# Performance work log

Measured on AMD Instinct MI355X. Metric: run time of the kernel, lower is better.

## Reference

```python
import jax, jax.numpy as jnp
import numpy as np

B, D, L, N, M, K = 256, 512, 196, 1024, 512, 10000  # batch, context, num_ctx, hidden, embed, vocab


def setup_inputs() -> dict:
    key = jax.random.key(0)
    ks = jax.random.split(key, 20)
    r = lambda k, s: jax.random.normal(k, s, dtype=jnp.float32) * 0.02
    return {
        "a_i": jax.random.normal(ks[0], (B, D, L), dtype=jnp.float32),
        "inp": jax.random.normal(ks[1], (B, 1, K), dtype=jnp.float32),
        "hn_prev": jax.random.normal(ks[2], (B, 1, N), dtype=jnp.float32),
        "cn_prev": jax.random.normal(ks[3], (B, 1, N), dtype=jnp.float32),
        "f_att_w": r(ks[4], (N + D,)),  # Linear(n+D -> 1), stored as a vector
        "f_att_b": r(ks[5], (1,)),
        "gate_w": r(ks[6], (N,)),       # Linear(n -> 1)
        "gate_b": r(ks[7], (1,)),
        "E_w": r(ks[8], (M, K)),        # torch Linear weight [out, in]
        "E_b": r(ks[9], (M,)),
        "W_ih": r(ks[10], (4 * N, D + N + M)),  # LSTM input->hidden (i,f,g,o)
        "W_hh": r(ks[11], (4 * N, N)),
        "b_ih": r(ks[12], (4 * N,)),
        "b_hh": r(ks[13], (4 * N,)),
        "Lh_w": r(ks[14], (M, N)),
        "Lh_b": r(ks[15], (M,)),
        "Lz_w": r(ks[16], (M, D)),
        "Lz_b": r(ks[17], (M,)),
        "Lo_w": r(ks[18], (K, M)),
        "Lo_b": r(ks[19], (K,)),
    }


def reference(a_i, inp, hn_prev, cn_prev,
              f_att_w, f_att_b, gate_w, gate_b,
              E_w, E_b, W_ih, W_hh, b_ih, b_hh,
              Lh_w, Lh_b, Lz_w, Lz_b, Lo_w, Lo_b):
    h = hn_prev[:, 0]  # [B, N]
    c = cn_prev[:, 0]  # [B, N]
    # --- additive attention: the 196-iteration torch loop batched into one einsum ---
    # cat((a_i[:,:,i], h)) @ f_att_w splits into the a-part and h-part of the weight.
    w_a, w_h = f_att_w[:D], f_att_w[D:]
    e = jnp.einsum('bdl,d->bl', a_i, w_a) + (h @ w_h)[:, None] + f_att_b  # [B, L]
    alpha = jax.nn.softmax(e, axis=1)                                     # [B, L]
    beta = jax.nn.sigmoid(h @ gate_w + gate_b)                            # [B]
    z = beta[:, None] * jnp.einsum('bl,bdl->bd', alpha, a_i)              # [B, D]
    # --- word embedding ---
    w_emb = inp[:, 0] @ E_w.T + E_b                                       # [B, M]
    # --- single-step LSTM (PyTorch gate order i, f, g, o) ---
    x = jnp.concatenate([w_emb, h, z], axis=1)                            # [B, M+N+D]
    gates = x @ W_ih.T + b_ih + h @ W_hh.T + b_hh                         # [B, 4N]
    i_g, f_g, g_g, o_g = jnp.split(gates, 4, axis=1)
    cn = jax.nn.sigmoid(f_g) * c + jax.nn.sigmoid(i_g) * jnp.tanh(g_g)
    hn = jax.nn.sigmoid(o_g) * jnp.tanh(cn)
    # --- output projection ---
    deep_out = w_emb + (hn @ Lh_w.T + Lh_b) + (z @ Lz_w.T + Lz_b)         # [B, M]
    p_yt = deep_out @ Lo_w.T + Lo_b                                       # [B, K]
    return (p_yt[:, None, :], hn[:, None, :], cn[:, None, :], alpha[:, None, :])
```

## Files before the change

### kernel.cpp

```cpp
#include <hip/hip_runtime.h>
#include <hip/hip_bf16.h>
#include <math.h>

#define BB 256
#define DD 512
#define LL 196
#define NN 1024
#define MM 512
#define KK 10000

#define OUT_PY 0
#define OUT_HN ((size_t)2560000)
#define OUT_CN ((size_t)2822144)
#define OUT_AL ((size_t)3084288)

#define OFF_PE     ((size_t)0)
#define OFF_BETA   ((size_t)802816)
#define OFF_Z      ((size_t)803072)
#define OFF_EMB    ((size_t)934144)
#define OFF_DEEP   ((size_t)1065216)
#define OFF_EMBP   ((size_t)1196288)
#define OFF_GATESP ((size_t)5390592)
#define OFF_DP     ((size_t)13779200)

typedef __attribute__((ext_vector_type(8))) short short8v;
typedef __attribute__((ext_vector_type(4))) float f32x4;

__device__ __forceinline__ unsigned short f2bf(float f) {
    unsigned int u = __builtin_bit_cast(unsigned int, f);
    u += 0x7fffu + ((u >> 16) & 1u);
    return (unsigned short)(u >> 16);
}

__device__ __forceinline__ void gl_lds16(const float* g, float* l) {
    __builtin_amdgcn_global_load_lds(
        (const __attribute__((address_space(1))) void*)g,
        (__attribute__((address_space(3))) void*)l, 16, 0, 0);
}

__device__ __forceinline__ short8v stage8(const float* __restrict__ p, bool ok,
                                          int kbase, int Ktot) {
    short8v v;
    if (ok && (kbase + 7 < Ktot)) {
        const float4 x = *(const float4*)(p + kbase);
        const float4 y = *(const float4*)(p + kbase + 4);
        v[0] = (short)f2bf(x.x); v[1] = (short)f2bf(x.y);
        v[2] = (short)f2bf(x.z); v[3] = (short)f2bf(x.w);
        v[4] = (short)f2bf(y.x); v[5] = (short)f2bf(y.y);
        v[6] = (short)f2bf(y.z); v[7] = (short)f2bf(y.w);
    } else {
#pragma unroll
        for (int i = 0; i < 8; ++i) {
            const int k = kbase + i;
            v[i] = (short)f2bf((ok && k < Ktot) ? p[k] : 0.f);
        }
    }
    return v;
}

struct GSrc { const float* A; int lda; const float* B; int ldb; int ktn; int K; };

__device__ __forceinline__ void gemm_body(
    const int bx, const int by, const int bz, const int rowBlocks,
    const GSrc s1, const GSrc s2,
    float* __restrict__ C, const int ldc, const int Ncols,
    const int ktPerSplit, const float* __restrict__ bias,
    short (*As)[64][72], short (*Bs)[64][72])
{
    const int t = threadIdx.x;
    const int row0 = bx * 64;
    const int col0 = by * 64;
    const int ktTot = s1.ktn + s2.ktn;
    const int kt0 = bz * ktPerSplit;
    const int nk = min(ktTot, kt0 + ktPerSplit) - kt0;

    const int sr = t >> 2;
    const int sk = (t & 3) << 4;
    const int bc = col0 + sr;
    const bool bok = (bc < Ncols);
    const float* aP1 = s1.A + (size_t)(row0 + sr) * s1.lda;
    const float* bP1 = s1.B + (size_t)(bok ? bc : 0) * s1.ldb;
    const float* aP2 = s2.A ? (s2.A + (size_t)(row0 + sr) * s2.lda) : aP1;
    const float* bP2 = s2.A ? (s2.B + (size_t)(bok ? bc : 0) * s2.ldb) : bP1;

    const int l = t & 63, w = t >> 6;
    const int wrow = (w >> 1) * 32, wcol = (w & 1) * 32;
    const int lr = l & 15, g = l >> 4, g8 = g * 8;

    f32x4 acc[2][2] = {};

    short8v sa0, sa1, sb0, sb1;
    {
        const int ktg = kt0;
        const float* aR; const float* bR; int kk, Kt;
        if (ktg < s1.ktn) { aR = aP1; bR = bP1; kk = (ktg << 6) + sk; Kt = s1.K; }
        else              { aR = aP2; bR = bP2; kk = ((ktg - s1.ktn) << 6) + sk; Kt = s2.K; }
        sa0 = stage8(aR, true, kk, Kt);  sa1 = stage8(aR, true, kk + 8, Kt);
        sb0 = stage8(bR, bok,  kk, Kt);  sb1 = stage8(bR, bok,  kk + 8, Kt);
    }
    *(short8v*)&As[0][sr][sk] = sa0; *(short8v*)&As[0][sr][sk + 8] = sa1;
    *(short8v*)&Bs[0][sr][sk] = sb0; *(short8v*)&Bs[0][sr][sk + 8] = sb1;
    __syncthreads();

    int cur = 0;
    for (int kt = 0; kt < nk; ++kt) {
        const bool more = (kt + 1 < nk);
        if (more) {
            const int ktg = kt0 + kt + 1;
            const float* aR; const float* bR; int kk, Kt;
            if (ktg < s1.ktn) { aR = aP1; bR = bP1; kk = (ktg << 6) + sk; Kt = s1.K; }
            else              { aR = aP2; bR = bP2; kk = ((ktg - s1.ktn) << 6) + sk; Kt = s2.K; }
            sa0 = stage8(aR, true, kk, Kt);  sa1 = stage8(aR, true, kk + 8, Kt);
            sb0 = stage8(bR, bok,  kk, Kt);  sb1 = stage8(bR, bok,  kk + 8, Kt);
        }
#pragma unroll
        for (int ks = 0; ks < 2; ++ks) {
            const int ko = ks * 32 + g8;
            short8v a0 = *(const short8v*)&As[cur][wrow + lr][ko];
            short8v a1 = *(const short8v*)&As[cur][wrow + 16 + lr][ko];
            short8v b0 = *(const short8v*)&Bs[cur][wcol + lr][ko];
            short8v b1 = *(const short8v*)&Bs[cur][wcol + 16 + lr][ko];
            acc[0][0] = __builtin_amdgcn_mfma_f32_16x16x32_bf16(a0, b0, acc[0][0], 0, 0, 0);
            acc[0][1] = __builtin_amdgcn_mfma_f32_16x16x32_bf16(a0, b1, acc[0][1], 0, 0, 0);
            acc[1][0] = __builtin_amdgcn_mfma_f32_16x16x32_bf16(a1, b0, acc[1][0], 0, 0, 0);
            acc[1][1] = __builtin_amdgcn_mfma_f32_16x16x32_bf16(a1, b1, acc[1][1], 0, 0, 0);
        }
        if (more) {
            *(short8v*)&As[cur ^ 1][sr][sk] = sa0;
            *(short8v*)&As[cur ^ 1][sr][sk + 8] = sa1;
            *(short8v*)&Bs[cur ^ 1][sr][sk] = sb0;
            *(short8v*)&Bs[cur ^ 1][sr][sk + 8] = sb1;
        }
        __syncthreads();
        cur ^= 1;
    }

    float* Cp = C + (size_t)bz * ((size_t)rowBlocks * 64) * ldc;
#pragma unroll
    for (int m = 0; m < 2; ++m)
#pragma unroll
        for (int n = 0; n < 2; ++n)
#pragma unroll
            for (int j = 0; j < 4; ++j) {
                const int r = row0 + wrow + m * 16 + g * 4 + j;
                const int c = col0 + wcol + n * 16 + lr;
                if (c < Ncols) {
                    float v = acc[m][n][j];
                    if (bias) v += bias[c];
                    Cp[(size_t)r * ldc + c] = v;
                }
            }
}

__global__ __launch_bounds__(256) void att_e_slab(
    const float* __restrict__ a_i, const float* __restrict__ f_att_w,
    float* __restrict__ pe)
{
    __shared__ __align__(16) float slab[6280];
    const int t = threadIdx.x;
    const int b = blockIdx.x >> 4, ch = blockIdx.x & 15;
    const int w = t >> 6, lane = t & 63;
    const float* gbase = a_i + ((size_t)b * DD + ch * 32) * LL;
#pragma unroll
    for (int k = 0; k < 7; ++k) {
        const int cw = k * 256 + w * 64;
        if (cw + lane < 1568)
            gl_lds16(gbase + (size_t)(cw + lane) * 4, slab + (size_t)cw * 4);
    }
    if (t < 8) slab[6272 + t] = 0.f;
    asm volatile("s_waitcnt vmcnt(0)" ::: "memory");
    __syncthreads();
    if (t < LL) {
        const float* wp = f_att_w + ch * 32;
        float e = 0.f;
#pragma unroll
        for (int d = 0; d < 32; ++d) e += slab[d * LL + t] * wp[d];
        pe[((size_t)b * 16 + ch) * LL + t] = e;
    }
}

__global__ __launch_bounds__(256) void att_z_slab(
    const float* __restrict__ a_i, const float* __restrict__ alpha,
    const float* __restrict__ beta, float* __restrict__ z)
{
    __shared__ __align__(16) float slab[6280];
    __shared__ float al[200];
    const int t = threadIdx.x;
    const int b = blockIdx.x >> 4, ch = blockIdx.x & 15;
    const int w = t >> 6, lane = t & 63;
    const float* gbase = a_i + ((size_t)b * DD + ch * 32) * LL;
#pragma unroll
    for (int k = 0; k < 7; ++k) {
        const int cw = k * 256 + w * 64;
        if (cw + lane < 1568)
            gl_lds16(gbase + (size_t)(cw + lane) * 4, slab + (size_t)cw * 4);
    }
    if (t < 200) al[t] = (t < LL) ? alpha[(size_t)b * LL + t] : 0.f;
    if (t < 8) slab[6272 + t] = 0.f;
    asm volatile("s_waitcnt vmcnt(0)" ::: "memory");
    __syncthreads();
    const int r = t >> 3, q = t & 7;
    const float* rowp = slab + r * LL + q * 25;
    const float* alq  = al + q * 25;
    float s = 0.f;
#pragma unroll
    for (int j = 0; j < 25; ++j) s += rowp[j] * alq[j];
    s += __shfl_xor(s, 1, 64);
    s += __shfl_xor(s, 2, 64);
    s += __shfl_xor(s, 4, 64);
    if (q == 0) z[(size_t)b * DD + ch * 32 + r] = beta[b] * s;
}

__global__ __launch_bounds__(256) void l2_emb_gatesh(
    const float* __restrict__ inp, const float* __restrict__ E_w,
    float* __restrict__ embp,
    const float* __restrict__ h, const float* __restrict__ W_ih,
    const float* __restrict__ W_hh, float* __restrict__ gatesp)
{
    __shared__ __align__(16) short As[2][64][72];
    __shared__ __align__(16) short Bs[2][64][72];
    const int bid = blockIdx.x;
    if (bid < 1024) {
        GSrc s1 = {inp, KK, E_w, KK, 157, KK};
        GSrc s2 = {nullptr, 0, nullptr, 0, 0, 0};
        gemm_body(bid & 3, (bid >> 2) & 7, bid >> 5, 4, s1, s2,
                  embp, MM, MM, 5, nullptr, As, Bs);
    } else {
        const int i = bid - 1024;
        GSrc s1 = {h, NN, W_ih + 512, 2048, 16, NN};
        GSrc s2 = {h, NN, W_hh, NN, 16, NN};
        gemm_body(i & 3, (i >> 2) & 63, i >> 8, 4, s1, s2,
                  gatesp, 4096, 4096, 8, nullptr, As, Bs);
    }
}

__global__ __launch_bounds__(256) void l3_softmax_embred(
    const float* __restrict__ pe, const float* __restrict__ h,
    const float* __restrict__ f_att_w, const float* __restrict__ f_att_b,
    const float* __restrict__ gate_w, const float* __restrict__ gate_b,
    float* __restrict__ alpha_out, float* __restrict__ beta,
    const float* __restrict__ embp, const float* __restrict__ E_b,
    float* __restrict__ emb)
{
    const int bid = blockIdx.x;
    const int t = threadIdx.x;
    if (bid < 256) {
        const int b = bid;
        __shared__ float red[256];
        __shared__ float red2[256];
        const float4 h4 = *(const float4*)(h + (size_t)b * NN + t * 4);
        const float4 w4 = *(const float4*)(f_att_w + DD + t * 4);
        const float4 g4 = *(const float4*)(gate_w + t * 4);
        float hd = h4.x * w4.x + h4.y * w4.y + h4.z * w4.z + h4.w * w4.w;
        float gd = h4.x * g4.x + h4.y * g4.y + h4.z * g4.z + h4.w * g4.w;
        red[t] = hd; red2[t] = gd;
        __syncthreads();
        for (int s = 128; s > 0; s >>= 1) {
            if (t < s) { red[t] += red[t + s]; red2[t] += red2[t + s]; }
            __syncthreads();
        }
        const float hdot = red[0];
        const float gdot = red2[0];
        __syncthreads();
        float e = -3.4e38f;
        if (t < LL) {
            const float* p = pe + (size_t)b * 16 * LL + t;
            e = hdot + f_att_b[0];
#pragma unroll
            for (int ch = 0; ch < 16; ++ch) e += p[ch * LL];
        }
        red[t] = e;
        __syncthreads();
        for (int s = 128; s > 0; s >>= 1) {
            if (t < s) red[t] = fmaxf(red[t], red[t + s]);
            __syncthreads();
        }
        const float mx = red[0];
        __syncthreads();
        const float ex = (t < LL) ? expf(e - mx) : 0.f;
        red[t] = ex;
        __syncthreads();
        for (int s = 128; s > 0; s >>= 1) {
            if (t < s) red[t] += red[t + s];
            __syncthreads();
        }
        const float inv = 1.f / red[0];
        if (t < LL) alpha_out[(size_t)b * LL + t] = ex * inv;
        if (t == 0) beta[b] = 1.f / (1.f + expf(-(gdot + gate_b[0])));
    } else {
        const int idx = (bid - 256) * 256 + t;
        const int j = idx & 511;
        float v = E_b[j];
#pragma unroll
        for (int s = 0; s < 32; ++s) v += embp[(size_t)s * (BB * 512) + idx];
        emb[idx] = v;
    }
}

__global__ __launch_bounds__(256) void l5_gatesez_lz(
    const float* __restrict__ emb, const float* __restrict__ z,
    const float* __restrict__ W_ih, float* __restrict__ gatesp,
    const float* __restrict__ Lz_w, float* __restrict__ dp)
{
    __shared__ __align__(16) short As[2][64][72];
    __shared__ __align__(16) short Bs[2][64][72];
    const int bid = blockIdx.x;
    if (bid < 512) {
        GSrc s1 = {emb, MM, W_ih, 2048, 8, MM};
        GSrc s2 = {nullptr, 0, nullptr, 0, 0, 0};
        gemm_body(bid & 3, (bid >> 2) & 63, bid >> 8, 4, s1, s2,
                  gatesp + (size_t)4 * BB * 4096, 4096, 4096, 4, nullptr, As, Bs);
    } else if (bid < 1024) {
        const int i = bid - 512;
        GSrc s1 = {z, DD, W_ih + 1536, 2048, 8, DD};
        GSrc s2 = {nullptr, 0, nullptr, 0, 0, 0};
        gemm_body(i & 3, (i >> 2) & 63, i >> 8, 4, s1, s2,
                  gatesp + (size_t)6 * BB * 4096, 4096, 4096, 4, nullptr, As, Bs);
    } else {
        const int i = bid - 1024;
        GSrc s1 = {z, DD, Lz_w, DD, 8, DD};
        GSrc s2 = {nullptr, 0, nullptr, 0, 0, 0};
        gemm_body(i & 3, (i >> 2) & 7, i >> 5, 4, s1, s2,
                  dp, MM, MM, 1, nullptr, As, Bs);
    }
}

__global__ __launch_bounds__(256) void l6_lstm(
    const float* __restrict__ gatesp,
    const float* __restrict__ b_ih, const float* __restrict__ b_hh,
    const float* __restrict__ c_prev, float* __restrict__ hn, float* __restrict__ cn)
{
    const int idx = blockIdx.x * 256 + threadIdx.x;
    const int b = idx >> 10, n = idx & 1023;
    float g[4];
#pragma unroll
    for (int gi = 0; gi < 4; ++gi) {
        const int col = gi * 1024 + n;
        const size_t o = (size_t)b * 4096 + col;
        float v = b_ih[col] + b_hh[col];
#pragma unroll
        for (int s = 0; s < 8; ++s) v += gatesp[(size_t)s * (BB * 4096) + o];
        g[gi] = v;
    }
    const float si = 1.f / (1.f + expf(-g[0]));
    const float sf = 1.f / (1.f + expf(-g[1]));
    const float so = 1.f / (1.f + expf(-g[3]));
    const float tg = tanhf(g[2]);
    const float c = c_prev[idx];
    const float cnv = sf * c + si * tg;
    const float hnv = so * tanhf(cnv);
    cn[idx] = cnv;
    hn[idx] = hnv;
}

__global__ __launch_bounds__(256) void l7_lh(
    const float* __restrict__ hn, const float* __restrict__ Lh_w,
    float* __restrict__ dp_hi)
{
    __shared__ __align__(16) short As[2][64][72];
    __shared__ __align__(16) short Bs[2][64][72];
    const int bid = blockIdx.x;
    GSrc s1 = {hn, NN, Lh_w, NN, 16, NN};
    GSrc s2 = {nullptr, 0, nullptr, 0, 0, 0};
    gemm_body(bid & 3, (bid >> 2) & 7, bid >> 5, 4, s1, s2,
              dp_hi, MM, MM, 1, nullptr, As, Bs);
}

__global__ __launch_bounds__(256) void l8_deep(
    const float* __restrict__ emb, const float* __restrict__ dp,
    const float* __restrict__ Lh_b, const float* __restrict__ Lz_b,
    float* __restrict__ deep)
{
    const int idx = blockIdx.x * 256 + threadIdx.x;
    const int j = idx & 511;
    float v = emb[idx] + Lh_b[j] + Lz_b[j];
#pragma unroll
    for (int s = 0; s < 24; ++s) v += dp[(size_t)s * (BB * 512) + idx];
    deep[idx] = v;
}

__global__ __launch_bounds__(256) void l9_pyt(
    const float* __restrict__ deep, const float* __restrict__ Lo_w,
    const float* __restrict__ Lo_b, float* __restrict__ out)
{
    __shared__ __align__(16) short As[2][64][72];
    __shared__ __align__(16) short Bs[2][64][72];
    const int bid = blockIdx.x;
    GSrc s1 = {deep, MM, Lo_w, MM, 8, MM};
    GSrc s2 = {nullptr, 0, nullptr, 0, 0, 0};
    gemm_body(bid & 3, bid >> 2, 0, 4, s1, s2,
              out, KK, KK, 8, Lo_b, As, Bs);
}

extern "C" void kernel_launch(void* const* d_in, const int* in_sizes, int n_in,
                              void* d_out, int out_size, void* d_ws, size_t ws_size,
                              hipStream_t stream)
{
    const float* a_i     = (const float*)d_in[0];
    const float* inp     = (const float*)d_in[1];
    const float* hn_prev = (const float*)d_in[2];
    const float* cn_prev = (const float*)d_in[3];
    const float* f_att_w = (const float*)d_in[4];
    const float* f_att_b = (const float*)d_in[5];
    const float* gate_w  = (const float*)d_in[6];
    const float* gate_b  = (const float*)d_in[7];
    const float* E_w     = (const float*)d_in[8];
    const float* E_b     = (const float*)d_in[9];
    const float* W_ih    = (const float*)d_in[10];
    const float* W_hh    = (const float*)d_in[11];
    const float* b_ih    = (const float*)d_in[12];
    const float* b_hh    = (const float*)d_in[13];
    const float* Lh_w    = (const float*)d_in[14];
    const float* Lh_b    = (const float*)d_in[15];
    const float* Lz_w    = (const float*)d_in[16];
    const float* Lz_b    = (const float*)d_in[17];
    const float* Lo_w    = (const float*)d_in[18];
    const float* Lo_b    = (const float*)d_in[19];

    float* out = (float*)d_out;
    float* ws  = (float*)d_ws;

    float* PE     = ws + OFF_PE;
    float* BETA   = ws + OFF_BETA;
    float* Z      = ws + OFF_Z;
    float* EMB    = ws + OFF_EMB;
    float* DEEP   = ws + OFF_DEEP;
    float* EMBP   = ws + OFF_EMBP;
    float* GATESP = ws + OFF_GATESP;
    float* DP     = ws + OFF_DP;

    att_e_slab<<<4096, 256, 0, stream>>>(a_i, f_att_w, PE);

    l2_emb_gatesh<<<2048, 256, 0, stream>>>(inp, E_w, EMBP,
                                            hn_prev, W_ih, W_hh, GATESP);

    l3_softmax_embred<<<768, 256, 0, stream>>>(PE, hn_prev, f_att_w, f_att_b,
                                               gate_w, gate_b, out + OUT_AL, BETA,
                                               EMBP, E_b, EMB);

    att_z_slab<<<4096, 256, 0, stream>>>(a_i, out + OUT_AL, BETA, Z);

    l5_gatesez_lz<<<1280, 256, 0, stream>>>(EMB, Z, W_ih, GATESP, Lz_w, DP);

    l6_lstm<<<1024, 256, 0, stream>>>(GATESP, b_ih, b_hh, cn_prev,
                                      out + OUT_HN, out + OUT_CN);

    l7_lh<<<512, 256, 0, stream>>>(out + OUT_HN, Lh_w,
                                   DP + (size_t)8 * BB * 512);

    l8_deep<<<512, 256, 0, stream>>>(EMB, DP, Lh_b, Lz_b, DEEP);

    l9_pyt<<<628, 256, 0, stream>>>(DEEP, Lo_w, Lo_b, out + OUT_PY);
}
```

Baseline: 156.7 us.

## Pre-convert GEMM operands to bf16 in a fused pass alongside attention scores

Adds a conversion pass, merged into the attention-score kernel as extra blocks, that writes bf16 copies of all weights and activations to workspace. Intermediate activations (emb, z, hn, deep) are also emitted as bf16, so every GEMM loads 16-byte bf16 vectors instead of converting fp32 inside the inner loop. The embedding GEMM's split-K factor is halved (fewer partials to reduce). The weight conversion runs every call, adding a full read of the fp32 weights plus a bf16 write and re-read, in exchange for halving operand traffic and removing per-tile conversion work.

```diff
diff --git a/kernel.cpp b/kernel.cpp
--- a/kernel.cpp
+++ b/kernel.cpp
@@ -16,12 +16,22 @@
 
 #define OFF_PE     ((size_t)0)
 #define OFF_BETA   ((size_t)802816)
-#define OFF_Z      ((size_t)803072)
-#define OFF_EMB    ((size_t)934144)
-#define OFF_DEEP   ((size_t)1065216)
-#define OFF_EMBP   ((size_t)1196288)
-#define OFF_GATESP ((size_t)5390592)
-#define OFF_DP     ((size_t)13779200)
+#define OFF_EMB    ((size_t)803072)
+#define OFF_EMBP   ((size_t)934144)
+#define OFF_GATESP ((size_t)3031296)
+#define OFF_DP     ((size_t)11419904)
+#define OFF_EWB    ((size_t)14565632)
+#define OFF_WIHB   ((size_t)17125632)
+#define OFF_WHHB   ((size_t)21319936)
+#define OFF_LHB    ((size_t)23417088)
+#define OFF_LZB    ((size_t)23679232)
+#define OFF_LOB    ((size_t)23810304)
+#define OFF_INPB   ((size_t)26370304)
+#define OFF_HB     ((size_t)27650304)
+#define OFF_ZB     ((size_t)27781376)
+#define OFF_EMBB   ((size_t)27846912)
+#define OFF_DEEPB  ((size_t)27912448)
+#define OFF_HNB    ((size_t)27977984)
 
 typedef __attribute__((ext_vector_type(8))) short short8v;
 typedef __attribute__((ext_vector_type(4))) float f32x4;
@@ -38,27 +48,19 @@
         (__attribute__((address_space(3))) void*)l, 16, 0, 0);
 }
 
-__device__ __forceinline__ short8v stage8(const float* __restrict__ p, bool ok,
-                                          int kbase, int Ktot) {
+__device__ __forceinline__ short8v stage8b(const unsigned short* __restrict__ p,
+                                           bool ok, int kbase, int Ktot) {
+    if (ok && (kbase + 7 < Ktot)) return *(const short8v*)(p + kbase);
     short8v v;
-    if (ok && (kbase + 7 < Ktot)) {
-        const float4 x = *(const float4*)(p + kbase);
-        const float4 y = *(const float4*)(p + kbase + 4);
-        v[0] = (short)f2bf(x.x); v[1] = (short)f2bf(x.y);
-        v[2] = (short)f2bf(x.z); v[3] = (short)f2bf(x.w);
-        v[4] = (short)f2bf(y.x); v[5] = (short)f2bf(y.y);
-        v[6] = (short)f2bf(y.z); v[7] = (short)f2bf(y.w);
-    } else {
-#pragma unroll
-        for (int i = 0; i < 8; ++i) {
-            const int k = kbase + i;
-            v[i] = (short)f2bf((ok && k < Ktot) ? p[k] : 0.f);
-        }
+#pragma unroll
+    for (int i = 0; i < 8; ++i) {
+        const int k = kbase + i;
+        v[i] = (ok && k < Ktot) ? (short)p[k] : (short)0;
     }
     return v;
 }
 
-struct GSrc { const float* A; int lda; const float* B; int ldb; int ktn; int K; };
+struct GSrc { const unsigned short* A; int lda; const unsigned short* B; int ldb; int ktn; int K; };
 
 __device__ __forceinline__ void gemm_body(
     const int bx, const int by, const int bz, const int rowBlocks,
@@ -78,10 +80,10 @@
     const int sk = (t & 3) << 4;
     const int bc = col0 + sr;
     const bool bok = (bc < Ncols);
-    const float* aP1 = s1.A + (size_t)(row0 + sr) * s1.lda;
-    const float* bP1 = s1.B + (size_t)(bok ? bc : 0) * s1.ldb;
-    const float* aP2 = s2.A ? (s2.A + (size_t)(row0 + sr) * s2.lda) : aP1;
-    const float* bP2 = s2.A ? (s2.B + (size_t)(bok ? bc : 0) * s2.ldb) : bP1;
+    const unsigned short* aP1 = s1.A + (size_t)(row0 + sr) * s1.lda;
+    const unsigned short* bP1 = s1.B + (size_t)(bok ? bc : 0) * s1.ldb;
+    const unsigned short* aP2 = s2.A ? (s2.A + (size_t)(row0 + sr) * s2.lda) : aP1;
+    const unsigned short* bP2 = s2.A ? (s2.B + (size_t)(bok ? bc : 0) * s2.ldb) : bP1;
 
     const int l = t & 63, w = t >> 6;
     const int wrow = (w >> 1) * 32, wcol = (w & 1) * 32;
@@ -92,11 +94,11 @@
     short8v sa0, sa1, sb0, sb1;
     {
         const int ktg = kt0;
-        const float* aR; const float* bR; int kk, Kt;
+        const unsigned short* aR; const unsigned short* bR; int kk, Kt;
         if (ktg < s1.ktn) { aR = aP1; bR = bP1; kk = (ktg << 6) + sk; Kt = s1.K; }
         else              { aR = aP2; bR = bP2; kk = ((ktg - s1.ktn) << 6) + sk; Kt = s2.K; }
-        sa0 = stage8(aR, true, kk, Kt);  sa1 = stage8(aR, true, kk + 8, Kt);
-        sb0 = stage8(bR, bok,  kk, Kt);  sb1 = stage8(bR, bok,  kk + 8, Kt);
+        sa0 = stage8b(aR, true, kk, Kt);  sa1 = stage8b(aR, true, kk + 8, Kt);
+        sb0 = stage8b(bR, bok,  kk, Kt);  sb1 = stage8b(bR, bok,  kk + 8, Kt);
     }
     *(short8v*)&As[0][sr][sk] = sa0; *(short8v*)&As[0][sr][sk + 8] = sa1;
     *(short8v*)&Bs[0][sr][sk] = sb0; *(short8v*)&Bs[0][sr][sk + 8] = sb1;
@@ -107,11 +109,11 @@
         const bool more = (kt + 1 < nk);
         if (more) {
             const int ktg = kt0 + kt + 1;
-            const float* aR; const float* bR; int kk, Kt;
+            const unsigned short* aR; const unsigned short* bR; int kk, Kt;
             if (ktg < s1.ktn) { aR = aP1; bR = bP1; kk = (ktg << 6) + sk; Kt = s1.K; }
             else              { aR = aP2; bR = bP2; kk = ((ktg - s1.ktn) << 6) + sk; Kt = s2.K; }
-            sa0 = stage8(aR, true, kk, Kt);  sa1 = stage8(aR, true, kk + 8, Kt);
-            sb0 = stage8(bR, bok,  kk, Kt);  sb1 = stage8(bR, bok,  kk + 8, Kt);
+            sa0 = stage8b(aR, true, kk, Kt);  sa1 = stage8b(aR, true, kk + 8, Kt);
+            sb0 = stage8b(bR, bok,  kk, Kt);  sb1 = stage8b(bR, bok,  kk + 8, Kt);
         }
 #pragma unroll
         for (int ks = 0; ks < 2; ++ks) {
@@ -152,83 +154,89 @@
             }
 }
 
-__global__ __launch_bounds__(256) void att_e_slab(
+#define CVT_NBLK 1615
+__global__ __launch_bounds__(256) void l1_atte_cvt(
     const float* __restrict__ a_i, const float* __restrict__ f_att_w,
-    float* __restrict__ pe)
+    float* __restrict__ pe,
+    const float* __restrict__ E_w, const float* __restrict__ W_ih,
+    const float* __restrict__ W_hh, const float* __restrict__ Lh_w,
+    const float* __restrict__ Lz_w, const float* __restrict__ Lo_w,
+    const float* __restrict__ inp, const float* __restrict__ h,
+    unsigned short* __restrict__ ewb, unsigned short* __restrict__ wihb,
+    unsigned short* __restrict__ whhb, unsigned short* __restrict__ lhb,
+    unsigned short* __restrict__ lzb, unsigned short* __restrict__ lob,
+    unsigned short* __restrict__ inpb, unsigned short* __restrict__ hb)
 {
     __shared__ __align__(16) float slab[6280];
+    const int bid = blockIdx.x;
     const int t = threadIdx.x;
-    const int b = blockIdx.x >> 4, ch = blockIdx.x & 15;
-    const int w = t >> 6, lane = t & 63;
-    const float* gbase = a_i + ((size_t)b * DD + ch * 32) * LL;
-#pragma unroll
-    for (int k = 0; k < 7; ++k) {
-        const int cw = k * 256 + w * 64;
-        if (cw + lane < 1568)
-            gl_lds16(gbase + (size_t)(cw + lane) * 4, slab + (size_t)cw * 4);
-    }
-    if (t < 8) slab[6272 + t] = 0.f;
-    asm volatile("s_waitcnt vmcnt(0)" ::: "memory");
-    __syncthreads();
-    if (t < LL) {
-        const float* wp = f_att_w + ch * 32;
-        float e = 0.f;
-#pragma unroll
-        for (int d = 0; d < 32; ++d) e += slab[d * LL + t] * wp[d];
-        pe[((size_t)b * 16 + ch) * LL + t] = e;
-    }
-}
-
-__global__ __launch_bounds__(256) void att_z_slab(
-    const float* __restrict__ a_i, const float* __restrict__ alpha,
-    const float* __restrict__ beta, float* __restrict__ z)
-{
-    __shared__ __align__(16) float slab[6280];
-    __shared__ float al[200];
-    const int t = threadIdx.x;
-    const int b = blockIdx.x >> 4, ch = blockIdx.x & 15;
-    const int w = t >> 6, lane = t & 63;
-    const float* gbase = a_i + ((size_t)b * DD + ch * 32) * LL;
-#pragma unroll
-    for (int k = 0; k < 7; ++k) {
-        const int cw = k * 256 + w * 64;
-        if (cw + lane < 1568)
-            gl_lds16(gbase + (size_t)(cw + lane) * 4, slab + (size_t)cw * 4);
-    }
-    if (t < 200) al[t] = (t < LL) ? alpha[(size_t)b * LL + t] : 0.f;
-    if (t < 8) slab[6272 + t] = 0.f;
-    asm volatile("s_waitcnt vmcnt(0)" ::: "memory");
-    __syncthreads();
-    const int r = t >> 3, q = t & 7;
-    const float* rowp = slab + r * LL + q * 25;
-    const float* alq  = al + q * 25;
-    float s = 0.f;
-#pragma unroll
-    for (int j = 0; j < 25; ++j) s += rowp[j] * alq[j];
-    s += __shfl_xor(s, 1, 64);
-    s += __shfl_xor(s, 2, 64);
-    s += __shfl_xor(s, 4, 64);
-    if (q == 0) z[(size_t)b * DD + ch * 32 + r] = beta[b] * s;
+
+    if (bid < 4096) {
+        const int b = bid >> 4, ch = bid & 15;
+        const int w = t >> 6, lane = t & 63;
+        const float* gbase = a_i + ((size_t)b * DD + ch * 32) * LL;
+#pragma unroll
+        for (int k = 0; k < 7; ++k) {
+            const int cw = k * 256 + w * 64;
+            if (cw + lane < 1568)
+                gl_lds16(gbase + (size_t)(cw + lane) * 4, slab + (size_t)cw * 4);
+        }
+        if (t < 8) slab[6272 + t] = 0.f;
+        asm volatile("s_waitcnt vmcnt(0)" ::: "memory");
+        __syncthreads();
+        if (t < LL) {
+            const float* wp = f_att_w + ch * 32;
+            float e = 0.f;
+#pragma unroll
+            for (int d = 0; d < 32; ++d) e += slab[d * LL + t] * wp[d];
+            pe[((size_t)b * 16 + ch) * LL + t] = e;
+        }
+    } else {
+        int lb = bid - 4096;
+        const float* src; unsigned short* dst; int n;
+        if      (lb < 313)  {             src = E_w;  dst = ewb;  n = 5120000; }
+        else if (lb < 825)  { lb -= 313;  src = W_ih; dst = wihb; n = 8388608; }
+        else if (lb < 1081) { lb -= 825;  src = W_hh; dst = whhb; n = 4194304; }
+        else if (lb < 1113) { lb -= 1081; src = Lh_w; dst = lhb;  n = 524288; }
+        else if (lb < 1129) { lb -= 1113; src = Lz_w; dst = lzb;  n = 262144; }
+        else if (lb < 1442) { lb -= 1129; src = Lo_w; dst = lob;  n = 5120000; }
+        else if (lb < 1599) { lb -= 1442; src = inp;  dst = inpb; n = 2560000; }
+        else                { lb -= 1599; src = h;    dst = hb;   n = 262144; }
+#pragma unroll
+        for (int i = 0; i < 8; ++i) {
+            const size_t e = (size_t)lb * 16384 + (size_t)i * 2048 + (size_t)t * 8;
+            if (e + 8 <= (size_t)n) {
+                const float4 x = *(const float4*)(src + e);
+                const float4 y = *(const float4*)(src + e + 4);
+                short8v v;
+                v[0] = (short)f2bf(x.x); v[1] = (short)f2bf(x.y);
+                v[2] = (short)f2bf(x.z); v[3] = (short)f2bf(x.w);
+                v[4] = (short)f2bf(y.x); v[5] = (short)f2bf(y.y);
+                v[6] = (short)f2bf(y.z); v[7] = (short)f2bf(y.w);
+                *(short8v*)(dst + e) = v;
+            }
+        }
+    }
 }
 
 __global__ __launch_bounds__(256) void l2_emb_gatesh(
-    const float* __restrict__ inp, const float* __restrict__ E_w,
+    const unsigned short* __restrict__ inpb, const unsigned short* __restrict__ ewb,
     float* __restrict__ embp,
-    const float* __restrict__ h, const float* __restrict__ W_ih,
-    const float* __restrict__ W_hh, float* __restrict__ gatesp)
+    const unsigned short* __restrict__ hb, const unsigned short* __restrict__ wihb,
+    const unsigned short* __restrict__ whhb, float* __restrict__ gatesp)
 {
     __shared__ __align__(16) short As[2][64][72];
     __shared__ __align__(16) short Bs[2][64][72];
     const int bid = blockIdx.x;
-    if (bid < 1024) {
-        GSrc s1 = {inp, KK, E_w, KK, 157, KK};
+    if (bid < 512) {
+        GSrc s1 = {inpb, KK, ewb, KK, 157, KK};
         GSrc s2 = {nullptr, 0, nullptr, 0, 0, 0};
         gemm_body(bid & 3, (bid >> 2) & 7, bid >> 5, 4, s1, s2,
-                  embp, MM, MM, 5, nullptr, As, Bs);
+                  embp, MM, MM, 10, nullptr, As, Bs);
     } else {
-        const int i = bid - 1024;
-        GSrc s1 = {h, NN, W_ih + 512, 2048, 16, NN};
-        GSrc s2 = {h, NN, W_hh, NN, 16, NN};
+        const int i = bid - 512;
+        GSrc s1 = {hb, NN, wihb + 512, 2048, 16, NN};
+        GSrc s2 = {hb, NN, whhb, NN, 16, NN};
         gemm_body(i & 3, (i >> 2) & 63, i >> 8, 4, s1, s2,
                   gatesp, 4096, 4096, 8, nullptr, As, Bs);
     }
@@ -240,7 +248,7 @@
     const float* __restrict__ gate_w, const float* __restrict__ gate_b,
     float* __restrict__ alpha_out, float* __restrict__ beta,
     const float* __restrict__ embp, const float* __restrict__ E_b,
-    float* __restrict__ emb)
+    float* __restrict__ emb, unsigned short* __restrict__ embb)
 {
     const int bid = blockIdx.x;
     const int t = threadIdx.x;
@@ -292,33 +300,66 @@
         const int j = idx & 511;
         float v = E_b[j];
 #pragma unroll
-        for (int s = 0; s < 32; ++s) v += embp[(size_t)s * (BB * 512) + idx];
+        for (int s = 0; s < 16; ++s) v += embp[(size_t)s * (BB * 512) + idx];
         emb[idx] = v;
-    }
+        embb[idx] = f2bf(v);
+    }
+}
+
+__global__ __launch_bounds__(256) void l4_attz(
+    const float* __restrict__ a_i, const float* __restrict__ alpha,
+    const float* __restrict__ beta, unsigned short* __restrict__ zb)
+{
+    __shared__ __align__(16) float slab[6280];
+    __shared__ float al[200];
+    const int t = threadIdx.x;
+    const int b = blockIdx.x >> 4, ch = blockIdx.x & 15;
+    const int w = t >> 6, lane = t & 63;
+    const float* gbase = a_i + ((size_t)b * DD + ch * 32) * LL;
+#pragma unroll
+    for (int k = 0; k < 7; ++k) {
+        const int cw = k * 256 + w * 64;
+        if (cw + lane < 1568)
+            gl_lds16(gbase + (size_t)(cw + lane) * 4, slab + (size_t)cw * 4);
+    }
+    if (t < 200) al[t] = (t < LL) ? alpha[(size_t)b * LL + t] : 0.f;
+    if (t < 8) slab[6272 + t] = 0.f;
+    asm volatile("s_waitcnt vmcnt(0)" ::: "memory");
+    __syncthreads();
+    const int r = t >> 3, q = t & 7;
+    const float* rowp = slab + r * LL + q * 25;
+    const float* alq  = al + q * 25;
+    float s = 0.f;
+#pragma unroll
+    for (int j = 0; j < 25; ++j) s += rowp[j] * alq[j];
+    s += __shfl_xor(s, 1, 64);
+    s += __shfl_xor(s, 2, 64);
+    s += __shfl_xor(s, 4, 64);
+    if (q == 0) zb[(size_t)b * DD + ch * 32 + r] = f2bf(beta[b] * s);
 }
 
 __global__ __launch_bounds__(256) void l5_gatesez_lz(
-    const float* __restrict__ emb, const float* __restrict__ z,
-    const float* __restrict__ W_ih, float* __restrict__ gatesp,
-    const float* __restrict__ Lz_w, float* __restrict__ dp)
+    const unsigned short* __restrict__ embb, const unsigned short* __restrict__ zb,
+    const unsigned short* __restrict__ wihb, float* __restrict__ gatesp,
+    const unsigned short* __restrict__ lzb, float* __restrict__ dp)
 {
     __shared__ __align__(16) short As[2][64][72];
     __shared__ __align__(16) short Bs[2][64][72];
     const int bid = blockIdx.x;
     if (bid < 512) {
-        GSrc s1 = {emb, MM, W_ih, 2048, 8, MM};
+        GSrc s1 = {embb, MM, wihb, 2048, 8, MM};
         GSrc s2 = {nullptr, 0, nullptr, 0, 0, 0};
         gemm_body(bid & 3, (bid >> 2) & 63, bid >> 8, 4, s1, s2,
                   gatesp + (size_t)4 * BB * 4096, 4096, 4096, 4, nullptr, As, Bs);
     } else if (bid < 1024) {
         const int i = bid - 512;
-        GSrc s1 = {z, DD, W_ih + 1536, 2048, 8, DD};
+        GSrc s1 = {zb, DD, wihb + 1536, 2048, 8, DD};
         GSrc s2 = {nullptr, 0, nullptr, 0, 0, 0};
         gemm_body(i & 3, (i >> 2) & 63, i >> 8, 4, s1, s2,
                   gatesp + (size_t)6 * BB * 4096, 4096, 4096, 4, nullptr, As, Bs);
     } else {
         const int i = bid - 1024;
-        GSrc s1 = {z, DD, Lz_w, DD, 8, DD};
+        GSrc s1 = {zb, DD, lzb, DD, 8, DD};
         GSrc s2 = {nullptr, 0, nullptr, 0, 0, 0};
         gemm_body(i & 3, (i >> 2) & 7, i >> 5, 4, s1, s2,
                   dp, MM, MM, 1, nullptr, As, Bs);
@@ -328,7 +369,8 @@
 __global__ __launch_bounds__(256) void l6_lstm(
     const float* __restrict__ gatesp,
     const float* __restrict__ b_ih, const float* __restrict__ b_hh,
-    const float* __restrict__ c_prev, float* __restrict__ hn, float* __restrict__ cn)
+    const float* __restrict__ c_prev, float* __restrict__ hn, float* __restrict__ cn,
+    unsigned short* __restrict__ hnb)
 {
     const int idx = blockIdx.x * 256 + threadIdx.x;
     const int b = idx >> 10, n = idx & 1023;
@@ -351,16 +393,17 @@
     const float hnv = so * tanhf(cnv);
     cn[idx] = cnv;
     hn[idx] = hnv;
+    hnb[idx] = f2bf(hnv);
 }
 
 __global__ __launch_bounds__(256) void l7_lh(
-    const float* __restrict__ hn, const float* __restrict__ Lh_w,
+    const unsigned short* __restrict__ hnb, const unsigned short* __restrict__ lhb,
     float* __restrict__ dp_hi)
 {
     __shared__ __align__(16) short As[2][64][72];
     __shared__ __align__(16) short Bs[2][64][72];
     const int bid = blockIdx.x;
-    GSrc s1 = {hn, NN, Lh_w, NN, 16, NN};
+    GSrc s1 = {hnb, NN, lhb, NN, 16, NN};
     GSrc s2 = {nullptr, 0, nullptr, 0, 0, 0};
     gemm_body(bid & 3, (bid >> 2) & 7, bid >> 5, 4, s1, s2,
               dp_hi, MM, MM, 1, nullptr, As, Bs);
@@ -369,24 +412,24 @@
 __global__ __launch_bounds__(256) void l8_deep(
     const float* __restrict__ emb, const float* __restrict__ dp,
     const float* __restrict__ Lh_b, const float* __restrict__ Lz_b,
-    float* __restrict__ deep)
+    unsigned short* __restrict__ deepb)
 {
     const int idx = blockIdx.x * 256 + threadIdx.x;
     const int j = idx & 511;
     float v = emb[idx] + Lh_b[j] + Lz_b[j];
 #pragma unroll
     for (int s = 0; s < 24; ++s) v += dp[(size_t)s * (BB * 512) + idx];
-    deep[idx] = v;
+    deepb[idx] = f2bf(v);
 }
 
 __global__ __launch_bounds__(256) void l9_pyt(
-    const float* __restrict__ deep, const float* __restrict__ Lo_w,
+    const unsigned short* __restrict__ deepb, const unsigned short* __restrict__ lob,
     const float* __restrict__ Lo_b, float* __restrict__ out)
 {
     __shared__ __align__(16) short As[2][64][72];
     __shared__ __align__(16) short Bs[2][64][72];
     const int bid = blockIdx.x;
-    GSrc s1 = {deep, MM, Lo_w, MM, 8, MM};
+    GSrc s1 = {deepb, MM, lob, MM, 8, MM};
     GSrc s2 = {nullptr, 0, nullptr, 0, 0, 0};
     gemm_body(bid & 3, bid >> 2, 0, 4, s1, s2,
               out, KK, KK, 8, Lo_b, As, Bs);
@@ -422,33 +465,45 @@
 
     float* PE     = ws + OFF_PE;
     float* BETA   = ws + OFF_BETA;
-    float* Z      = ws + OFF_Z;
     float* EMB    = ws + OFF_EMB;
-    float* DEEP   = ws + OFF_DEEP;
     float* EMBP   = ws + OFF_EMBP;
     float* GATESP = ws + OFF_GATESP;
     float* DP     = ws + OFF_DP;
-
-    att_e_slab<<<4096, 256, 0, stream>>>(a_i, f_att_w, PE);
-
-    l2_emb_gatesh<<<2048, 256, 0, stream>>>(inp, E_w, EMBP,
-                                            hn_prev, W_ih, W_hh, GATESP);
+    unsigned short* EWB   = (unsigned short*)(ws + OFF_EWB);
+    unsigned short* WIHB  = (unsigned short*)(ws + OFF_WIHB);
+    unsigned short* WHHB  = (unsigned short*)(ws + OFF_WHHB);
+    unsigned short* LHB   = (unsigned short*)(ws + OFF_LHB);
+    unsigned short* LZB   = (unsigned short*)(ws + OFF_LZB);
+    unsigned short* LOB   = (unsigned short*)(ws + OFF_LOB);
+    unsigned short* INPB  = (unsigned short*)(ws + OFF_INPB);
+    unsigned short* HB    = (unsigned short*)(ws + OFF_HB);
+    unsigned short* ZB    = (unsigned short*)(ws + OFF_ZB);
+    unsigned short* EMBB  = (unsigned short*)(ws + OFF_EMBB);
+    unsigned short* DEEPB = (unsigned short*)(ws + OFF_DEEPB);
+    unsigned short* HNB   = (unsigned short*)(ws + OFF_HNB);
+
+    l1_atte_cvt<<<4096 + CVT_NBLK, 256, 0, stream>>>(
+        a_i, f_att_w, PE,
+        E_w, W_ih, W_hh, Lh_w, Lz_w, Lo_w, inp, hn_prev,
+        EWB, WIHB, WHHB, LHB, LZB, LOB, INPB, HB);
+
+    l2_emb_gatesh<<<1536, 256, 0, stream>>>(INPB, EWB, EMBP,
+                                            HB, WIHB, WHHB, GATESP);
 
     l3_softmax_embred<<<768, 256, 0, stream>>>(PE, hn_prev, f_att_w, f_att_b,
                                                gate_w, gate_b, out + OUT_AL, BETA,
-                                               EMBP, E_b, EMB);
-
-    att_z_slab<<<4096, 256, 0, stream>>>(a_i, out + OUT_AL, BETA, Z);
-
-    l5_gatesez_lz<<<1280, 256, 0, stream>>>(EMB, Z, W_ih, GATESP, Lz_w, DP);
+                                               EMBP, E_b, EMB, EMBB);
+
+    l4_attz<<<4096, 256, 0, stream>>>(a_i, out + OUT_AL, BETA, ZB);
+
+    l5_gatesez_lz<<<1280, 256, 0, stream>>>(EMBB, ZB, WIHB, GATESP, LZB, DP);
 
     l6_lstm<<<1024, 256, 0, stream>>>(GATESP, b_ih, b_hh, cn_prev,
-                                      out + OUT_HN, out + OUT_CN);
-
-    l7_lh<<<512, 256, 0, stream>>>(out + OUT_HN, Lh_w,
-                                   DP + (size_t)8 * BB * 512);
-
-    l8_deep<<<512, 256, 0, stream>>>(EMB, DP, Lh_b, Lz_b, DEEP);
-
-    l9_pyt<<<628, 256, 0, stream>>>(DEEP, Lo_w, Lo_b, out + OUT_PY);
-}
+                                      out + OUT_HN, out + OUT_CN, HNB);
+
+    l7_lh<<<512, 256, 0, stream>>>(HNB, LHB, DP + (size_t)8 * BB * 512);
+
+    l8_deep<<<512, 256, 0, stream>>>(EMB, DP, Lh_b, Lz_b, DEEPB);
+
+    l9_pyt<<<628, 256, 0, stream>>>(DEEPB, LOB, Lo_b, out + OUT_PY);
+}
```

Result: faster. 138.5 us (-11.6%).
